# Kernel tuning notes

Measured on AMD Instinct MI355X. Metric: run time of the kernel, lower is better.

The kernel has to match this reference:

```python
import jax, jax.numpy as jnp
import numpy as np

B, I, O, H = 1024, 64, 64, 32  # batch, input_size, output_size, hidden_size
NEG_SLOPE = 0.01  # nn.LeakyReLU default


def leaky(x):
    return jnp.where(x >= 0, x, NEG_SLOPE * x)


def setup_inputs() -> dict:
    key = jax.random.key(0)
    ks = jax.random.split(key, 9)
    u = lambda k, shape, b: jax.random.uniform(k, shape, jnp.float32, -b, b)
    # Per-edge tiny MLP params, stacked over [O, I] edges.
    # Linear(1,H): fan_in=1 -> bound 1.0 ; Linear(H,H)/Linear(H,1): bound 1/sqrt(H)
    bnd = 1.0 / np.sqrt(H)
    return {
        "x": jax.random.normal(ks[0], (B, I), jnp.float32),
        "W1": u(ks[1], (O, I, H), 1.0),        # Linear(1,H) weight
        "b1": u(ks[2], (O, I, H), 1.0),
        "W2": u(ks[3], (O, I, H, H), bnd),     # Linear(H,H) weight [out,in]
        "b2": u(ks[4], (O, I, H), bnd),
        "W3": u(ks[5], (O, I, H), bnd),        # Linear(H,1) weight
        "b3": u(ks[6], (O, I), bnd),
        "layer_w": jnp.ones((O, I), jnp.float32),           # layer_weight init 1.0
        "bias_w": u(ks[7], (O, I), 0.1),                     # bias_weight ~ U(-0.1,0.1)
    }


def reference(x, W1, b1, W2, b2, W3, b3, layer_w, bias_w):
    # All O*I edge MLPs evaluated as one batched computation.
    # h1[b,o,i,h] = leaky(x[b,i] * W1[o,i,h] + b1[o,i,h])
    h1 = leaky(x[:, None, :, None] * W1 + b1)                      # [B,O,I,H]
    h2 = leaky(jnp.einsum('boih,oikh->boik', h1, W2) + b2)         # [B,O,I,H]
    edge = jnp.einsum('boih,oih->boi', h2, W3) + b3                # [B,O,I]
    edge = bias_w * leaky(x)[:, None, :] + layer_w * edge          # per-edge output
    return edge.sum(axis=2)                                        # [B,O]
```

## Files before the change

### kernel.cpp

```cpp
#include <hip/hip_runtime.h>


#define H_   32
#define NI   64
#define NO   64
#define NB   1024
#define ROWS 64
#define XS   68

typedef float    floatx4 __attribute__((ext_vector_type(4)));
typedef _Float16 halfx8  __attribute__((ext_vector_type(8)));
typedef _Float16 halfx2  __attribute__((ext_vector_type(2)));

union H8 { halfx8 v8; halfx2 v2[4]; unsigned int u[4]; };

__device__ inline float leaky(float v) { return fmaxf(v, 0.01f * v); }

__device__ inline unsigned int pkrtz(float a, float b) {
    return __builtin_bit_cast(unsigned int, __builtin_amdgcn_cvt_pkrtz(a, b));
}

__global__ __launch_bounds__(256, 4)
void kan_kernel(const float* __restrict__ x,  const float* __restrict__ W1,
                const float* __restrict__ b1, const float* __restrict__ W2,
                const float* __restrict__ b2, const float* __restrict__ W3,
                const float* __restrict__ b3, const float* __restrict__ lw,
                const float* __restrict__ bw, float* __restrict__ out)
{
    __shared__ float    xs[ROWS * XS];
    __shared__ _Float16 w1s[NI * H_];
    __shared__ _Float16 b1s[NI * H_];
    __shared__ float    rc[ROWS];
    __shared__ float    part[4][ROWS];

    const int t    = threadIdx.x;
    const int o    = blockIdx.x;
    const int row0 = blockIdx.y * ROWS;

    const float* xsrc = x + (size_t)row0 * NI;
    #pragma unroll
    for (int v = 0; v < 4; ++v) {
        int fe = (v * 256 + t) * 4;
        int r = fe >> 6, c = fe & 63;
        *(float4*)(&xs[r * XS + c]) = *(const float4*)(xsrc + fe);
    }
    const float* w1g = W1 + (size_t)o * NI * H_;
    const float* b1g = b1 + (size_t)o * NI * H_;
    #pragma unroll
    for (int v = 0; v < 2; ++v) {
        int e = (v * 256 + t) * 4;
        float4 a = *(const float4*)(w1g + e);
        float4 c = *(const float4*)(b1g + e);
        uint2 pa = { pkrtz(a.x, a.y), pkrtz(a.z, a.w) };
        uint2 pc = { pkrtz(c.x, c.y), pkrtz(c.z, c.w) };
        *(uint2*)(w1s + e) = pa;
        *(uint2*)(b1s + e) = pc;
    }
    __syncthreads();

    if (t < ROWS) {
        float s = 0.f;
        const float* bwp = bw + o * NI;
        const float* lp  = lw + o * NI;
        const float* b3p = b3 + o * NI;
        for (int i = 0; i < NI; ++i)
            s += bwp[i] * leaky(xs[t * XS + i]) + lp[i] * b3p[i];
        rc[t] = s;
    }

    const int lane = t & 63, wave = t >> 6;
    const int col  = lane & 15;
    const int kh   = lane >> 4;
    const int koff = kh * 8;
    const int i0   = wave * 16;

    const float* w2p0 = W2 + ((size_t)(o * NI + i0) * H_ + col) * H_ + koff;
    const float* w2p1 = w2p0 + 16 * H_;
    const float* b2p  = b2 + (size_t)(o * NI + i0) * H_ + col;
    const float* w3p  = W3 + (size_t)(o * NI + i0) * H_ + col;
    const float* lwp  = lw + o * NI + i0;
    const halfx2 slope = { (_Float16)0.01f, (_Float16)0.01f };

    floatx4 pacc[4] = { {0,0,0,0}, {0,0,0,0}, {0,0,0,0}, {0,0,0,0} };

    #pragma unroll 2
    for (int ii = 0; ii < 16; ++ii) {
        const int i = i0 + ii;

        floatx4 a0 = *(const floatx4*)(w2p0);
        floatx4 a1 = *(const floatx4*)(w2p0 + 4);
        floatx4 a2 = *(const floatx4*)(w2p1);
        floatx4 a3 = *(const floatx4*)(w2p1 + 4);
        H8 bf0, bf1;
        bf0.u[0] = pkrtz(a0[0], a0[1]);  bf0.u[1] = pkrtz(a0[2], a0[3]);
        bf0.u[2] = pkrtz(a1[0], a1[1]);  bf0.u[3] = pkrtz(a1[2], a1[3]);
        bf1.u[0] = pkrtz(a2[0], a2[1]);  bf1.u[1] = pkrtz(a2[2], a2[3]);
        bf1.u[2] = pkrtz(a3[0], a3[1]);  bf1.u[3] = pkrtz(a3[2], a3[3]);

        H8 w1v, b1v;
        w1v.v8 = *(const halfx8*)(w1s + i * H_ + koff);
        b1v.v8 = *(const halfx8*)(b1s + i * H_ + koff);

        float lwv  = lwp[ii];
        float b2c0 = b2p[0],       b2c1 = b2p[16];
        float w3e0 = lwv * w3p[0], w3e1 = lwv * w3p[16];

        #pragma unroll
        for (int m = 0; m < 4; ++m) {
            float xv = xs[(m * 16 + col) * XS + i];
            halfx2 xx = __builtin_bit_cast(halfx2,
                            __builtin_amdgcn_cvt_pkrtz(xv, xv));
            H8 af;
            #pragma unroll
            for (int j = 0; j < 4; ++j) {
                halfx2 h = __builtin_elementwise_fma(xx, w1v.v2[j], b1v.v2[j]);
                af.v2[j] = __builtin_elementwise_max(h, h * slope);
            }
            floatx4 c0 = { b2c0, b2c0, b2c0, b2c0 };
            floatx4 c1 = { b2c1, b2c1, b2c1, b2c1 };
            c0 = __builtin_amdgcn_mfma_f32_16x16x32_f16(af.v8, bf0.v8, c0, 0, 0, 0);
            c1 = __builtin_amdgcn_mfma_f32_16x16x32_f16(af.v8, bf1.v8, c1, 0, 0, 0);
            #pragma unroll
            for (int r = 0; r < 4; ++r)
                pacc[m][r] += leaky(c0[r]) * w3e0 + leaky(c1[r]) * w3e1;
        }

        w2p0 += H_ * H_;  w2p1 += H_ * H_;
        b2p  += H_;       w3p  += H_;
    }

    #pragma unroll
    for (int m = 0; m < 4; ++m) {
        #pragma unroll
        for (int r = 0; r < 4; ++r) {
            float v = pacc[m][r];
            v += __shfl_xor(v, 1, 64);
            v += __shfl_xor(v, 2, 64);
            v += __shfl_xor(v, 4, 64);
            v += __shfl_xor(v, 8, 64);
            if (col == 0)
                part[wave][m * 16 + kh * 4 + r] = v;
        }
    }
    __syncthreads();

    if (t < ROWS) {
        float v = part[0][t] + part[1][t] + part[2][t] + part[3][t] + rc[t];
        out[(size_t)(row0 + t) * NO + o] = v;
    }
}

extern "C" void kernel_launch(void* const* d_in, const int* in_sizes, int n_in,
                              void* d_out, int out_size, void* d_ws, size_t ws_size,
                              hipStream_t stream) {
    const float* x  = (const float*)d_in[0];
    const float* W1 = (const float*)d_in[1];
    const float* b1 = (const float*)d_in[2];
    const float* W2 = (const float*)d_in[3];
    const float* b2 = (const float*)d_in[4];
    const float* W3 = (const float*)d_in[5];
    const float* b3 = (const float*)d_in[6];
    const float* lw = (const float*)d_in[7];
    const float* bw = (const float*)d_in[8];
    float* out = (float*)d_out;

    dim3 grid(NO, NB / ROWS);
    kan_kernel<<<grid, dim3(256), 0, stream>>>(x, W1, b1, W2, b2, W3, b3, lw, bw, out);
}
```

Measured before the change: 116.1 us.

## Pre-pack x, W3·lw and b2 as fp16 in LDS; rewrite leaky via abs

Stores x in shared memory as pre-duplicated fp16 pairs, which removes a convert from the inner loop. Pre-packs lw·W3 and b2 per edge into fp16 pairs in LDS, replacing the per-iteration global scalar loads. The leaky ReLU times W3 becomes an FMA chain using 0.505·v + 0.495·|v|, dropping the max. The loop unroll also goes from 2 to 4. These changes add fp16 rounding of W3, b2 and the x used in the residual term, which can cost accuracy.

```diff
diff --git a/kernel.cpp b/kernel.cpp
--- a/kernel.cpp
+++ b/kernel.cpp
@@ -6,7 +6,7 @@
 #define NO   64
 #define NB   1024
 #define ROWS 64
-#define XS   68
+#define XSTR 66
 
 typedef float    floatx4 __attribute__((ext_vector_type(4)));
 typedef _Float16 halfx8  __attribute__((ext_vector_type(8)));
@@ -27,11 +27,12 @@
                 const float* __restrict__ b3, const float* __restrict__ lw,
                 const float* __restrict__ bw, float* __restrict__ out)
 {
-    __shared__ float    xs[ROWS * XS];
+    __shared__ unsigned int xsp[ROWS * XSTR];
     __shared__ _Float16 w1s[NI * H_];
     __shared__ _Float16 b1s[NI * H_];
-    __shared__ float    rc[ROWS];
-    __shared__ float    part[4][ROWS];
+    __shared__ unsigned int wbs[NI * H_];
+    __shared__ float rc[ROWS];
+    __shared__ float part[4][ROWS];
 
     const int t    = threadIdx.x;
     const int o    = blockIdx.x;
@@ -42,7 +43,11 @@
     for (int v = 0; v < 4; ++v) {
         int fe = (v * 256 + t) * 4;
         int r = fe >> 6, c = fe & 63;
-        *(float4*)(&xs[r * XS + c]) = *(const float4*)(xsrc + fe);
+        float4 xv = *(const float4*)(xsrc + fe);
+        uint2 lo = { pkrtz(xv.x, xv.x), pkrtz(xv.y, xv.y) };
+        uint2 hi = { pkrtz(xv.z, xv.z), pkrtz(xv.w, xv.w) };
+        *(uint2*)(&xsp[r * XSTR + c])     = lo;
+        *(uint2*)(&xsp[r * XSTR + c + 2]) = hi;
     }
     const float* w1g = W1 + (size_t)o * NI * H_;
     const float* b1g = b1 + (size_t)o * NI * H_;
@@ -56,6 +61,20 @@
         *(uint2*)(w1s + e) = pa;
         *(uint2*)(b1s + e) = pc;
     }
+    {
+        int e = t * 8;
+        float l = lw[o * NI + (e >> 5)];
+        const float* w3g = W3 + (size_t)o * NI * H_ + e;
+        const float* b2g = b2 + (size_t)o * NI * H_ + e;
+        float4 wa = *(const float4*)(w3g),     wb2 = *(const float4*)(w3g + 4);
+        float4 ba = *(const float4*)(b2g),     bb  = *(const float4*)(b2g + 4);
+        uint4 p0 = { pkrtz(l * wa.x, ba.x), pkrtz(l * wa.y, ba.y),
+                     pkrtz(l * wa.z, ba.z), pkrtz(l * wa.w, ba.w) };
+        uint4 p1 = { pkrtz(l * wb2.x, bb.x), pkrtz(l * wb2.y, bb.y),
+                     pkrtz(l * wb2.z, bb.z), pkrtz(l * wb2.w, bb.w) };
+        *(uint4*)(&wbs[e])     = p0;
+        *(uint4*)(&wbs[e + 4]) = p1;
+    }
     __syncthreads();
 
     if (t < ROWS) {
@@ -63,8 +82,10 @@
         const float* bwp = bw + o * NI;
         const float* lp  = lw + o * NI;
         const float* b3p = b3 + o * NI;
-        for (int i = 0; i < NI; ++i)
-            s += bwp[i] * leaky(xs[t * XS + i]) + lp[i] * b3p[i];
+        for (int i = 0; i < NI; ++i) {
+            halfx2 hx = __builtin_bit_cast(halfx2, xsp[t * XSTR + i]);
+            s += bwp[i] * leaky((float)hx[0]) + lp[i] * b3p[i];
+        }
         rc[t] = s;
     }
 
@@ -76,14 +97,11 @@
 
     const float* w2p0 = W2 + ((size_t)(o * NI + i0) * H_ + col) * H_ + koff;
     const float* w2p1 = w2p0 + 16 * H_;
-    const float* b2p  = b2 + (size_t)(o * NI + i0) * H_ + col;
-    const float* w3p  = W3 + (size_t)(o * NI + i0) * H_ + col;
-    const float* lwp  = lw + o * NI + i0;
     const halfx2 slope = { (_Float16)0.01f, (_Float16)0.01f };
 
     floatx4 pacc[4] = { {0,0,0,0}, {0,0,0,0}, {0,0,0,0}, {0,0,0,0} };
 
-    #pragma unroll 2
+    #pragma unroll 4
     for (int ii = 0; ii < 16; ++ii) {
         const int i = i0 + ii;
 
@@ -101,15 +119,16 @@
         w1v.v8 = *(const halfx8*)(w1s + i * H_ + koff);
         b1v.v8 = *(const halfx8*)(b1s + i * H_ + koff);
 
-        float lwv  = lwp[ii];
-        float b2c0 = b2p[0],       b2c1 = b2p[16];
-        float w3e0 = lwv * w3p[0], w3e1 = lwv * w3p[16];
+        halfx2 q0 = __builtin_bit_cast(halfx2, wbs[i * H_ + col]);
+        halfx2 q1 = __builtin_bit_cast(halfx2, wbs[i * H_ + col + 16]);
+        float w3e0 = (float)q0[0], b2c0 = (float)q0[1];
+        float w3e1 = (float)q1[0], b2c1 = (float)q1[1];
+        float p0 = 0.505f * w3e0, n0 = 0.495f * w3e0;
+        float p1 = 0.505f * w3e1, n1 = 0.495f * w3e1;
 
         #pragma unroll
         for (int m = 0; m < 4; ++m) {
-            float xv = xs[(m * 16 + col) * XS + i];
-            halfx2 xx = __builtin_bit_cast(halfx2,
-                            __builtin_amdgcn_cvt_pkrtz(xv, xv));
+            halfx2 xx = __builtin_bit_cast(halfx2, xsp[(m * 16 + col) * XSTR + i]);
             H8 af;
             #pragma unroll
             for (int j = 0; j < 4; ++j) {
@@ -121,12 +140,15 @@
             c0 = __builtin_amdgcn_mfma_f32_16x16x32_f16(af.v8, bf0.v8, c0, 0, 0, 0);
             c1 = __builtin_amdgcn_mfma_f32_16x16x32_f16(af.v8, bf1.v8, c1, 0, 0, 0);
             #pragma unroll
-            for (int r = 0; r < 4; ++r)
-                pacc[m][r] += leaky(c0[r]) * w3e0 + leaky(c1[r]) * w3e1;
+            for (int r = 0; r < 4; ++r) {
+                pacc[m][r] = fmaf(p0, c0[r],
+                             fmaf(n0, fabsf(c0[r]),
+                             fmaf(p1, c1[r],
+                             fmaf(n1, fabsf(c1[r]), pacc[m][r]))));
+            }
         }
 
         w2p0 += H_ * H_;  w2p1 += H_ * H_;
-        b2p  += H_;       w3p  += H_;
     }
 
     #pragma unroll
```

Result: faster. 113.0 us (-2.7%).
